# Kernel tuning notes

Measured on AMD Instinct MI355X. Metric: run time of the kernel, lower is better.

## Reference

```python
import jax, jax.numpy as jnp
import numpy as np

N_STATE = 1024
N_HEAD = 16
D_K = N_STATE // N_HEAD  # 64


def setup_inputs() -> dict:
    key = jax.random.key(0)
    ks = jax.random.split(key, 12)
    B, S = 2, 2048
    s = 1.0 / np.sqrt(N_STATE)
    inp = {
        "q": jax.random.normal(ks[0], (B, S, N_STATE), jnp.float32),
        "k": jax.random.normal(ks[1], (B, S, N_STATE), jnp.float32),
        "v": jax.random.normal(ks[2], (B, S, N_STATE), jnp.float32),
        # Linear weights in torch layout [out_features, in_features]
        "Wq": jax.random.normal(ks[3], (N_STATE, N_STATE), jnp.float32) * s,
        "bq": jax.random.normal(ks[4], (N_STATE,), jnp.float32) * s,
        "Wk": jax.random.normal(ks[5], (N_STATE, N_STATE), jnp.float32) * s,
        "bk": jax.random.normal(ks[6], (N_STATE,), jnp.float32) * s,
        "Wv": jax.random.normal(ks[7], (N_STATE, N_STATE), jnp.float32) * s,
        "bv": jax.random.normal(ks[8], (N_STATE,), jnp.float32) * s,
        "Wo": jax.random.normal(ks[9], (N_STATE, N_STATE), jnp.float32) * s,
        "bo": jax.random.normal(ks[10], (N_STATE,), jnp.float32) * s,
    }
    return inp


def reference(q, k, v, Wq, bq, Wk, bk, Wv, bv, Wo, bo):
    B = q.shape[0]
    # projections (torch Linear: x @ W.T + b), split heads -> [B, H, S, d]
    def proj(x, W, b):
        y = jnp.einsum('bsi,oi->bso', x, W) + b
        return y.reshape(B, -1, N_HEAD, D_K).transpose(0, 2, 1, 3)
    qh = proj(q, Wq, bq)
    kh = proj(k, Wk, bk)
    vh = proj(v, Wv, bv)
    # scaled dot-product attention, full [B,H,Sq,Sk] scores as in original
    scores = jnp.einsum('bhqd,bhkd->bhqk', qh, kh) / np.sqrt(D_K).astype(np.float32)
    attn = jax.nn.softmax(scores, axis=-1)
    out = jnp.einsum('bhqk,bhkd->bhqd', attn, vh)
    out = out.transpose(0, 2, 1, 3).reshape(B, -1, N_HEAD * D_K)
    return jnp.einsum('bsi,oi->bso', out, Wo) + bo
```

## Files before the change

### kernel.cpp

```cpp
#include <hip/hip_runtime.h>
#include <stdint.h>

typedef __attribute__((ext_vector_type(8))) short short8;
typedef __attribute__((ext_vector_type(4))) float f32x4;
typedef __attribute__((ext_vector_type(4))) uint32_t u32x4;

#if __has_builtin(__builtin_amdgcn_exp2f)
#define EXP2(x) __builtin_amdgcn_exp2f(x)
#else
#define EXP2(x) exp2f(x)
#endif

__device__ __forceinline__ short f2bf(float f){
  uint32_t u = __builtin_bit_cast(uint32_t, f);
  return (short)((u + 0x8000u) >> 16);
}
__device__ __forceinline__ uint32_t pk2(float lo, float hi){
  uint32_t a = __builtin_bit_cast(uint32_t, lo) + 0x8000u;
  uint32_t b = __builtin_bit_cast(uint32_t, hi) + 0x8000u;
#if __has_builtin(__builtin_amdgcn_perm)
  return __builtin_amdgcn_perm(b, a, 0x07060302u);
#else
  return (b & 0xFFFF0000u) | (a >> 16);
#endif
}
__device__ __forceinline__ void gload16(const void* g, void* l){
  __builtin_amdgcn_global_load_lds((const __attribute__((address_space(1))) void*)g,
                                   (__attribute__((address_space(3))) void*)l, 16, 0, 0);
}

__global__ __launch_bounds__(512) void cvt_all(
    const float* __restrict__ q, const float* __restrict__ k, const float* __restrict__ v,
    const float* __restrict__ wq, const float* __restrict__ wk, const float* __restrict__ wv,
    const float* __restrict__ wo, short* __restrict__ dst){
  const size_t SQ = 4096ull*1024ull, NW = 1024ull*1024ull;
  size_t e = (size_t)(blockIdx.x*512u + threadIdx.x)*8ull;
  const float* src; size_t rel;
  if (e < 3*SQ){ size_t which = e / SQ; src = which==0?q:(which==1?k:v); rel = e - which*SQ; }
  else { size_t e2 = e - 3*SQ; size_t which = e2 / NW;
         src = which==0?wq:(which==1?wk:(which==2?wv:wo)); rel = e2 - which*NW; }
  float4 a = *(const float4*)(src + rel);
  float4 b = *(const float4*)(src + rel + 4);
  u32x4 r = { pk2(a.x,a.y), pk2(a.z,a.w), pk2(b.x,b.y), pk2(b.z,b.w) };
  *(u32x4*)(dst + e) = r;
}

template<int MODE>
__device__ __forceinline__ void gemm_body(const short* __restrict__ A, const short* __restrict__ Bw,
    const float* __restrict__ bias, void* __restrict__ Cout, float scale, int m0, int n0){
  const int K = 1024;
  __shared__ short Al[128*64];
  __shared__ short Bl[64*64];
  int tid = threadIdx.x;
  int w = tid >> 6, lane = tid & 63, lr = lane & 15, lg = lane >> 4;
  int wr = w >> 1, wc = w & 1;
  f32x4 acc[2][2] = {};
  int row0 = tid >> 3;
  int qc0  = (tid & 7) ^ (row0 & 7);
  const short* Ag = A  + (size_t)(m0 + row0)*K + qc0*8;
  const short* Bg = Bw + (size_t)(n0 + row0)*K + qc0*8;
  char* Alb = (char*)Al + tid*16;
  char* Blb = (char*)Bl + tid*16;
  int ra[2], rb[2];
#pragma unroll
  for (int mi=0; mi<2; ++mi){ int r = wr*32 + mi*16 + lr; ra[mi] = r; }
#pragma unroll
  for (int ni=0; ni<2; ++ni){ int r = wc*32 + ni*16 + lr; rb[ni] = r; }
  for (int k0 = 0; k0 < K; k0 += 64){
    gload16(Ag + k0,                Alb);
    gload16(Ag + k0 + 64*(size_t)K, Alb + 8192);
    gload16(Bg + k0,                Blb);
    __syncthreads();
#pragma unroll
    for (int kk=0; kk<2; ++kk){
      short8 av[2], bv[2];
#pragma unroll
      for (int mi=0; mi<2; ++mi)
        av[mi] = *(const short8*)((char*)Al + ra[mi]*128 + (((kk*4 + lg) ^ (ra[mi] & 7)) << 4));
#pragma unroll
      for (int ni=0; ni<2; ++ni)
        bv[ni] = *(const short8*)((char*)Bl + rb[ni]*128 + (((kk*4 + lg) ^ (rb[ni] & 7)) << 4));
#pragma unroll
      for (int mi=0; mi<2; ++mi)
#pragma unroll
        for (int ni=0; ni<2; ++ni)
          acc[mi][ni] = __builtin_amdgcn_mfma_f32_16x16x32_bf16(av[mi], bv[ni], acc[mi][ni], 0, 0, 0);
    }
    __syncthreads();
  }
#pragma unroll
  for (int ni=0; ni<2; ++ni){
    int col = n0 + wc*32 + ni*16 + lr;
    float bb = bias[col];
#pragma unroll
    for (int mi=0; mi<2; ++mi){
#pragma unroll
      for (int i2=0; i2<4; ++i2){
        int row = m0 + wr*32 + mi*16 + lg*4 + i2;
        float val = (acc[mi][ni][i2] + bb) * scale;
        if (MODE == 0){
          int b = row >> 11, s = row & 2047, h = col >> 6, d = col & 63;
          ((short*)Cout)[(((size_t)(b*16 + h))*2048 + s)*64 + d] = f2bf(val);
        } else {
          ((float*)Cout)[(size_t)row*1024 + col] = val;
        }
      }
    }
  }
}

__global__ __launch_bounds__(512) void gemm_qkv(
    const short* __restrict__ qb, const short* __restrict__ kb, const short* __restrict__ vb,
    const short* __restrict__ Wqb, const short* __restrict__ Wkb, const short* __restrict__ Wvb,
    const float* __restrict__ bq, const float* __restrict__ bk, const float* __restrict__ bv,
    short* __restrict__ Qh, short* __restrict__ Kh, short* __restrict__ Vh, float qscale){
  int f = (blockIdx.z*32 + blockIdx.y)*16 + blockIdx.x;
  int L = (f & 7)*192 + (f >> 3);
  int z = L >> 9, r = L & 511;
  int m0 = (r >> 4)*128, n0 = (r & 15)*64;
  const short* A  = z==0 ? qb  : (z==1 ? kb  : vb);
  const short* Bw = z==0 ? Wqb : (z==1 ? Wkb : Wvb);
  const float* bi = z==0 ? bq  : (z==1 ? bk  : bv);
  short* C        = z==0 ? Qh  : (z==1 ? Kh  : Vh);
  float s = z==0 ? qscale : 1.0f;
  gemm_body<0>(A, Bw, bi, (void*)C, s, m0, n0);
}

__global__ __launch_bounds__(512) void gemm_out(const short* __restrict__ A, const short* __restrict__ Bw,
    const float* __restrict__ bias, float* __restrict__ Cout){
  int f = blockIdx.y*gridDim.x + blockIdx.x;
  int L = (f & 7)*64 + (f >> 3);
  int m0 = (L >> 4)*128, n0 = (L & 15)*64;
  gemm_body<1>(A, Bw, bias, (void*)Cout, 1.0f, m0, n0);
}

__global__ __launch_bounds__(512) void attn_fwd(const short* __restrict__ Qh, const short* __restrict__ Kh,
    const short* __restrict__ Vh, short* __restrict__ AO){
  const int S = 2048;
  int i = blockIdx.y*gridDim.x + blockIdx.x;
  int L = (i & 7)*64 + (i >> 3);
  int bh = L >> 4, qt = L & 15;
  __shared__ short Kl[2][64*64];
  __shared__ short Vt[2][64*72];
  int tid = threadIdx.x, w = tid >> 6, lane = tid & 63, lr = lane & 15, lg = lane >> 4;
  const short* Qb = Qh + (size_t)bh*S*64;
  const short* Kb = Kh + (size_t)bh*S*64;
  const short* Vb = Vh + (size_t)bh*S*64;
  int q0 = qt*128 + w*16;
  short8 aq[2];
#pragma unroll
  for (int h=0; h<2; ++h)
    aq[h] = *(const short8*)&Qb[(size_t)(q0 + lr)*64 + h*32 + lg*8];
  f32x4 o[4] = {};
  float lsum = 0.f;
  int koff = tid*16;
  int kr = tid >> 3, kc = tid & 7;
  int ksw = (kr & 3) | (((kr >> 3) & 1) << 2);
  int ksrc = kr*64 + ((kc ^ ksw) << 3);
  int Rbase = 8*(lr >> 2) + (lr & 3);
  int sR = (lr & 3) | (((lr >> 2) & 1) << 2);
  int slot0 = (lg ^ sR) << 3, slot1 = ((lg + 4) ^ sR) << 3;
  int vr = tid >> 3;
  int d0 = (tid & 7)*8;
  int c0 = vr ^ d0;
  gload16(Kb + ksrc, (char*)&Kl[0][0] + koff);
  {
    short8 v0 = *(const short8*)&Vb[(size_t)vr*64 + d0];
#pragma unroll
    for (int j=0; j<8; ++j) Vt[0][(d0 + j)*72 + c0] = v0[j];
  }
  __syncthreads();

  for (int t = 0; t < 32; ++t){
    int buf = t & 1, nbuf = buf ^ 1;
    short8 nv;
    bool pre = (t + 1 < 32);
    if (pre){
      gload16(Kb + (size_t)(t + 1)*4096 + ksrc, (char*)&Kl[nbuf][0] + koff);
      nv = *(const short8*)&Vb[(size_t)((t + 1)*64 + vr)*64 + d0];
    }
    const short* Kbuf = &Kl[buf][0];
    uint32_t Wp[2][2][2];
#pragma unroll
    for (int nf=0; nf<4; ++nf){
      int R = Rbase + (nf & 1)*4 + (nf >> 1)*32;
      short8 ak0 = *(const short8*)&Kbuf[R*64 + slot0];
      short8 ak1 = *(const short8*)&Kbuf[R*64 + slot1];
      f32x4 z = {};
      z = __builtin_amdgcn_mfma_f32_16x16x32_bf16(ak0, aq[0], z, 0, 0, 0);
      z = __builtin_amdgcn_mfma_f32_16x16x32_bf16(ak1, aq[1], z, 0, 0, 0);
      float p0 = EXP2(z[0]), p1 = EXP2(z[1]);
      float p2 = EXP2(z[2]), p3 = EXP2(z[3]);
      lsum += (p0 + p1) + (p2 + p3);
      Wp[nf >> 1][nf & 1][0] = pk2(p0, p1);
      Wp[nf >> 1][nf & 1][1] = pk2(p2, p3);
    }
    short8 pa[2];
#pragma unroll
    for (int c=0; c<2; ++c){
      union { uint32_t u[4]; short8 s; } tt;
      tt.u[0] = Wp[c][0][0]; tt.u[1] = Wp[c][0][1];
      tt.u[2] = Wp[c][1][0]; tt.u[3] = Wp[c][1][1];
      pa[c] = tt.s;
    }
    const short* Vbuf = &Vt[buf][0];
#pragma unroll
    for (int df=0; df<4; ++df){
      int h = (df*2 + (lr >> 3)) & 7;
      int rowv = (df*16 + lr)*72;
      short8 vb0 = *(const short8*)&Vbuf[rowv + ((lg ^ h) << 3)];
      short8 vb1 = *(const short8*)&Vbuf[rowv + (((lg + 4) ^ h) << 3)];
      o[df] = __builtin_amdgcn_mfma_f32_16x16x32_bf16(pa[0], vb0, o[df], 0, 0, 0);
      o[df] = __builtin_amdgcn_mfma_f32_16x16x32_bf16(pa[1], vb1, o[df], 0, 0, 0);
    }
    if (pre){
#pragma unroll
      for (int j=0; j<8; ++j) Vt[nbuf][(d0 + j)*72 + c0] = nv[j];
    }
    __syncthreads();
  }
  lsum += __shfl_xor(lsum, 16); lsum += __shfl_xor(lsum, 32);
  int b = bh >> 4, hh = bh & 15;
  float rinv[4];
#pragma unroll
  for (int i2=0; i2<4; ++i2) rinv[i2] = 1.0f / __shfl(lsum, (lg << 2) + i2);
#pragma unroll
  for (int df=0; df<4; ++df)
#pragma unroll
    for (int i2=0; i2<4; ++i2){
      int row = q0 + lg*4 + i2;
      int col = df*16 + lr;
      AO[((size_t)(b*2048 + row))*1024 + hh*64 + col] = f2bf(o[df][i2] * rinv[i2]);
    }
}

extern "C" void kernel_launch(void* const* d_in, const int* in_sizes, int n_in,
                              void* d_out, int out_size, void* d_ws, size_t ws_size,
                              hipStream_t stream){
  const float* q  = (const float*)d_in[0];
  const float* k  = (const float*)d_in[1];
  const float* v  = (const float*)d_in[2];
  const float* Wq = (const float*)d_in[3];
  const float* bq = (const float*)d_in[4];
  const float* Wk = (const float*)d_in[5];
  const float* bk = (const float*)d_in[6];
  const float* Wv = (const float*)d_in[7];
  const float* bv = (const float*)d_in[8];
  const float* Wo = (const float*)d_in[9];
  const float* bo = (const float*)d_in[10];

  const size_t SQ = 4096ull*1024ull, NW = 1024ull*1024ull;
  short* ws  = (short*)d_ws;
  short* qb  = ws;
  short* kb  = ws + SQ;
  short* vb  = ws + 2*SQ;
  short* Wqb = ws + 3*SQ;
  short* Wkb = Wqb + NW;
  short* Wvb = Wkb + NW;
  short* Wob = Wvb + NW;
  short* Qh  = Wob + NW;
  short* Kh  = Qh + SQ;
  short* Vh  = Kh + SQ;
  short* AO  = qb;

  const float Csc = 0.18033688011112042f;

  cvt_all<<<4096, 512, 0, stream>>>(q, k, v, Wq, Wk, Wv, Wo, ws);
  gemm_qkv<<<dim3(16, 32, 3), 512, 0, stream>>>(qb, kb, vb, Wqb, Wkb, Wvb, bq, bk, bv, Qh, Kh, Vh, Csc);
  attn_fwd<<<dim3(16, 32), 512, 0, stream>>>(Qh, Kh, Vh, AO);
  gemm_out<<<dim3(16, 32), 512, 0, stream>>>(AO, Wob, bo, (float*)d_out);
}
```

Measured before the change: 123.9 us.

## Triple-buffer K tiles with partial vmcnt waits and MFMA priority hints

After: 118.6 us. -4.3%, faster.

```diff
diff --git a/kernel.cpp b/kernel.cpp
--- a/kernel.cpp
+++ b/kernel.cpp
@@ -140,7 +140,7 @@
   int i = blockIdx.y*gridDim.x + blockIdx.x;
   int L = (i & 7)*64 + (i >> 3);
   int bh = L >> 4, qt = L & 15;
-  __shared__ short Kl[2][64*64];
+  __shared__ short Kl[3][4096];
   __shared__ short Vt[2][64*72];
   int tid = threadIdx.x, w = tid >> 6, lane = tid & 63, lr = lane & 15, lg = lane >> 4;
   const short* Qb = Qh + (size_t)bh*S*64;
@@ -163,24 +163,27 @@
   int vr = tid >> 3;
   int d0 = (tid & 7)*8;
   int c0 = vr ^ d0;
-  gload16(Kb + ksrc, (char*)&Kl[0][0] + koff);
+  gload16(Kb + ksrc,        (char*)&Kl[0][0] + koff);
+  gload16(Kb + 4096 + ksrc, (char*)&Kl[1][0] + koff);
   {
     short8 v0 = *(const short8*)&Vb[(size_t)vr*64 + d0];
 #pragma unroll
     for (int j=0; j<8; ++j) Vt[0][(d0 + j)*72 + c0] = v0[j];
   }
-  __syncthreads();
+  asm volatile("s_waitcnt vmcnt(1) lgkmcnt(0)" ::: "memory");
+  __builtin_amdgcn_sched_barrier(0);
+  __builtin_amdgcn_s_barrier();
 
   for (int t = 0; t < 32; ++t){
-    int buf = t & 1, nbuf = buf ^ 1;
+    int buf = t % 3;
     short8 nv;
-    bool pre = (t + 1 < 32);
-    if (pre){
-      gload16(Kb + (size_t)(t + 1)*4096 + ksrc, (char*)&Kl[nbuf][0] + koff);
+    if (t + 1 < 32)
       nv = *(const short8*)&Vb[(size_t)((t + 1)*64 + vr)*64 + d0];
-    }
+    if (t + 2 < 32)
+      gload16(Kb + (size_t)(t + 2)*4096 + ksrc, (char*)&Kl[(t + 2) % 3][0] + koff);
     const short* Kbuf = &Kl[buf][0];
     uint32_t Wp[2][2][2];
+    __builtin_amdgcn_s_setprio(1);
 #pragma unroll
     for (int nf=0; nf<4; ++nf){
       int R = Rbase + (nf & 1)*4 + (nf >> 1)*32;
@@ -195,6 +198,7 @@
       Wp[nf >> 1][nf & 1][0] = pk2(p0, p1);
       Wp[nf >> 1][nf & 1][1] = pk2(p2, p3);
     }
+    __builtin_amdgcn_s_setprio(0);
     short8 pa[2];
 #pragma unroll
     for (int c=0; c<2; ++c){
@@ -203,7 +207,8 @@
       tt.u[2] = Wp[c][1][0]; tt.u[3] = Wp[c][1][1];
       pa[c] = tt.s;
     }
-    const short* Vbuf = &Vt[buf][0];
+    const short* Vbuf = &Vt[t & 1][0];
+    __builtin_amdgcn_s_setprio(1);
 #pragma unroll
     for (int df=0; df<4; ++df){
       int h = (df*2 + (lr >> 3)) & 7;
@@ -213,11 +218,16 @@
       o[df] = __builtin_amdgcn_mfma_f32_16x16x32_bf16(pa[0], vb0, o[df], 0, 0, 0);
       o[df] = __builtin_amdgcn_mfma_f32_16x16x32_bf16(pa[1], vb1, o[df], 0, 0, 0);
     }
-    if (pre){
-#pragma unroll
-      for (int j=0; j<8; ++j) Vt[nbuf][(d0 + j)*72 + c0] = nv[j];
-    }
-    __syncthreads();
+    __builtin_amdgcn_s_setprio(0);
+    if (t + 1 < 32){
+      short* Vn = &Vt[(t + 1) & 1][0];
+#pragma unroll
+      for (int j=0; j<8; ++j) Vn[(d0 + j)*72 + c0] = nv[j];
+      if (t < 30) asm volatile("s_waitcnt vmcnt(1) lgkmcnt(0)" ::: "memory");
+      else        asm volatile("s_waitcnt vmcnt(0) lgkmcnt(0)" ::: "memory");
+      __builtin_amdgcn_sched_barrier(0);
+      __builtin_amdgcn_s_barrier();
+    }
   }
   lsum += __shfl_xor(lsum, 16); lsum += __shfl_xor(lsum, 32);
   int b = bh >> 4, hh = bh & 15;
```
